# Kernel optimization log

Hardware: AMD Instinct MI355X
Metric: run time of the kernel (lower is better)

The kernel has to match this reference:

```python
import jax, jax.numpy as jnp
import numpy as np

V, F, KIN, KSEL, VSEL = 200000, 128, 64, 16, 50000


def setup_inputs() -> dict:
    key = jax.random.key(0)
    k1, k2, k3, k4 = jax.random.split(key, 4)
    features = jax.random.normal(k1, (V, F), dtype=jnp.float32)
    distances = jax.random.uniform(k2, (V, KIN), dtype=jnp.float32)
    # -1 encodes 'missing neighbour' (as in HGCalML kNN convention); allow some -1s
    nidx = jax.random.randint(k3, (V, KIN), -1, V).astype(jnp.int32)
    # first neighbour is the vertex itself, at distance 0 (kNN convention)
    nidx = nidx.at[:, 0].set(jnp.arange(V, dtype=jnp.int32))
    distances = distances.at[:, 0].set(0.0)
    # cluster-centre selection indices (stand-in for LocalCluster custom-op output)
    sel_idx = jax.random.randint(k4, (VSEL, 1), 0, V).astype(jnp.int32)
    return {"features": features, "distances": distances, "nidx": nidx,
            "sel_idx": sel_idx, "K": KSEL}


def reference(features, distances, nidx, sel_idx, K):
    # --- SortAndSelectNeighbours.raw_call (radius < 0 => no radius cut) ---
    BIG = jnp.float32(1e9)
    tfdist = jnp.where(nidx < 0, BIG, distances)          # push missing to the end
    order = jnp.argsort(tfdist, axis=1)                   # [V, KIN]
    snidx = jnp.take_along_axis(nidx, order, axis=1)[:, :K]  # [V, K] int32

    # --- SelectFromIndices: apply cluster-centre selection ---
    sel_nidx = snidx[sel_idx[:, 0]]                       # [VSEL, K]

    # --- GraphClusterReshape.raw_call: gather, zero-pad mask, flatten ---
    safe_idx = jnp.where(sel_nidx < 0, 0, sel_nidx)       # -1 -> 0 for gather
    gfeat = features[safe_idx]                            # [VSEL, K, F]
    gfeat = jnp.where(sel_nidx[..., None] < 0, jnp.float32(0.0), gfeat)
    return gfeat.reshape(sel_idx.shape[0], K * features.shape[1])  # [VSEL, K*F]
```

## Files before the change

### kernel.cpp

```cpp
#include <hip/hip_runtime.h>
#include <stdint.h>

constexpr int V    = 200000;
constexpr int F    = 128;
constexpr int KIN  = 64;
constexpr int KSEL = 16;
constexpr int VSEL = 50000;

__global__ __launch_bounds__(256) void lcr_kernel(
    const float* __restrict__ features,
    const float* __restrict__ distances,
    const int*   __restrict__ nidx,
    const int*   __restrict__ sel_idx,
    float*       __restrict__ out)
{
    const int lane = threadIdx.x & 63;
    const int wave = threadIdx.x >> 6;
    const int row  = blockIdx.x * 4 + wave;
    if (row >= VSEL) return;

    const int v = sel_idx[row];

    const float d  = distances[(size_t)v * KIN + lane];
    const int   ni = nidx     [(size_t)v * KIN + lane];

    const uint32_t bits = __float_as_uint(ni < 0 ? 1.0e9f : d);
    uint64_t key = ((uint64_t)bits << 6) | (uint32_t)lane;

    #pragma unroll
    for (int k = 2; k <= 64; k <<= 1) {
        #pragma unroll
        for (int j = k >> 1; j >= 1; j >>= 1) {
            const uint64_t other = __shfl_xor(key, j, 64);
            const bool lower    = (lane & j) == 0;
            const bool asc      = (lane & k) == 0;
            const bool take_min = (lower == asc);
            const bool swap     = take_min ? (other < key) : (other > key);
            key = swap ? other : key;
        }
    }

    const int col       = (int)(key & 63);
    const int sorted_ni = __shfl(ni, col, 64);

    const size_t out_base = (size_t)row * (KSEL * F);
    #pragma unroll 4
    for (int kk = 0; kk < KSEL; ++kk) {
        const int idx = __shfl(sorted_ni, kk, 64);
        float2 val;
        if (idx < 0) {
            val.x = 0.0f; val.y = 0.0f;
        } else {
            val = *reinterpret_cast<const float2*>(
                      &features[(size_t)idx * F + lane * 2]);
        }
        *reinterpret_cast<float2*>(&out[out_base + (size_t)kk * F + lane * 2]) = val;
    }
}

extern "C" void kernel_launch(void* const* d_in, const int* in_sizes, int n_in,
                              void* d_out, int out_size, void* d_ws, size_t ws_size,
                              hipStream_t stream)
{
    const float* features  = (const float*)d_in[0];
    const float* distances = (const float*)d_in[1];
    const int*   nidx      = (const int*)  d_in[2];
    const int*   sel_idx   = (const int*)  d_in[3];
    float* out = (float*)d_out;

    const int rows_per_block = 4;
    const int grid = (VSEL + rows_per_block - 1) / rows_per_block;
    lcr_kernel<<<grid, 256, 0, stream>>>(features, distances, nidx, sel_idx, out);
}
```

Baseline: 155.6 us.

## Widen gather to 16-byte loads, batch all loads, use nontemporal stores

The gather is restructured so each half-wave handles one neighbour row with 16-byte vector loads, covering two rows per iteration. All eight loads are issued before any store to raise memory-level parallelism. Missing indices are clamped to zero and the result masked instead of branching. Output is written with nontemporal stores so it does not pollute the cache. This costs more registers per thread and adds loads of row 0 for missing neighbours.

```diff
diff --git a/kernel.cpp b/kernel.cpp
--- a/kernel.cpp
+++ b/kernel.cpp
@@ -1,11 +1,12 @@
 #include <hip/hip_runtime.h>
 #include <stdint.h>
 
-constexpr int V    = 200000;
 constexpr int F    = 128;
 constexpr int KIN  = 64;
 constexpr int KSEL = 16;
 constexpr int VSEL = 50000;
+
+typedef float f32x4 __attribute__((ext_vector_type(4)));
 
 __global__ __launch_bounds__(256) void lcr_kernel(
     const float* __restrict__ features,
@@ -43,18 +44,29 @@
     const int col       = (int)(key & 63);
     const int sorted_ni = __shfl(ni, col, 64);
 
+    const int half = lane >> 5;
+    const int l32  = lane & 31;
+
+    int idxs[8];
+    #pragma unroll
+    for (int p = 0; p < 8; ++p)
+        idxs[p] = __shfl(sorted_ni, 2 * p + half, 64);
+
+    f32x4 vals[8];
+    #pragma unroll
+    for (int p = 0; p < 8; ++p) {
+        const int safe = idxs[p] < 0 ? 0 : idxs[p];
+        vals[p] = *reinterpret_cast<const f32x4*>(
+                      &features[(size_t)safe * F + l32 * 4]);
+    }
+
     const size_t out_base = (size_t)row * (KSEL * F);
-    #pragma unroll 4
-    for (int kk = 0; kk < KSEL; ++kk) {
-        const int idx = __shfl(sorted_ni, kk, 64);
-        float2 val;
-        if (idx < 0) {
-            val.x = 0.0f; val.y = 0.0f;
-        } else {
-            val = *reinterpret_cast<const float2*>(
-                      &features[(size_t)idx * F + lane * 2]);
-        }
-        *reinterpret_cast<float2*>(&out[out_base + (size_t)kk * F + lane * 2]) = val;
+    #pragma unroll
+    for (int p = 0; p < 8; ++p) {
+        f32x4 val = vals[p];
+        if (idxs[p] < 0) { val = (f32x4)(0.0f); }
+        __builtin_nontemporal_store(val,
+            reinterpret_cast<f32x4*>(&out[out_base + (size_t)(2 * p + half) * F + l32 * 4]));
     }
 }
 
```

After: 127.2 us. 1.22x faster.
